# Kernel tuning notes

Hardware: AMD Instinct MI355X
Metric: run time of the kernel (lower is better)

## Reference

```python
import jax, jax.numpy as jnp
import numpy as np

B, S, D, H = 4, 1024, 1024, 16
HD = D // H  # head_dim = 64
NEG = -1e9  # stands in for float('-inf') in masked_fill; numerically safe


def setup_inputs() -> dict:
    key = jax.random.key(0)
    ks = jax.random.split(key, 8)
    q = jax.random.normal(ks[0], (B, S, D), dtype=jnp.float32)
    k = jax.random.normal(ks[1], (B, S, D), dtype=jnp.float32)
    v = jax.random.normal(ks[2], (B, S, D), dtype=jnp.float32)
    # padding mask: True marks padded positions; pad out the tail of each sequence
    pos = jnp.arange(S)
    lengths = jnp.array([S, S - 64, S - 128, S - 256])
    padding_mask = pos[None, :] >= lengths[:, None]  # [B, S] bool
    # additive causal mask: 0 on/below diagonal, NEG above
    causal_mask = jnp.where(jnp.tril(jnp.ones((S, S), dtype=bool)), 0.0, NEG).astype(jnp.float32)
    scale = 1.0 / np.sqrt(D)
    Wq = jax.random.normal(ks[3], (D, D), dtype=jnp.float32) * scale
    Wk = jax.random.normal(ks[4], (D, D), dtype=jnp.float32) * scale
    Wv = jax.random.normal(ks[5], (D, D), dtype=jnp.float32) * scale
    Wo = jax.random.normal(ks[6], (D, D), dtype=jnp.float32) * scale
    return {"q": q, "k": k, "v": v, "padding_mask": padding_mask,
            "causal_mask": causal_mask, "Wq": Wq, "Wk": Wk, "Wv": Wv,
            "Wo": Wo, "n_heads": H}


def reference(q, k, v, padding_mask, causal_mask, Wq, Wk, Wv, Wo, n_heads):
    b, s, d = q.shape
    hd = d // n_heads
    # projections (nn.Linear: x @ W^T, no bias)
    qp = (q @ Wq.T).reshape(b, s, n_heads, hd).transpose(0, 2, 1, 3)  # [b,h,s,hd]
    kp = (k @ Wk.T).reshape(b, s, n_heads, hd).transpose(0, 2, 1, 3)
    vp = (v @ Wv.T).reshape(b, s, n_heads, hd).transpose(0, 2, 1, 3)
    scores = jnp.einsum('bhqd,bhkd->bhqk', qp, kp) / jnp.sqrt(jnp.float32(hd))
    # masked_fill(padding_mask, -inf): mask broadcast over heads and query dim
    scores = jnp.where(padding_mask[:, None, None, :], NEG, scores)
    scores = scores + causal_mask  # additive causal mask
    attn = jax.nn.softmax(scores, axis=-1)
    out = jnp.einsum('bhqk,bhkd->bhqd', attn, vp)
    out = out.transpose(0, 2, 1, 3).reshape(b, s, d)
    return out @ Wo.T
```

## Files before the change

kernel.cpp:

```cpp
#include <hip/hip_runtime.h>
#include <hip/hip_bf16.h>

#define BB 4
#define SS 1024
#define DD 1024
#define HH 16
#define HD 64
#define MM (BB*SS)


typedef __bf16 bf16x8 __attribute__((ext_vector_type(8)));
typedef __bf16 bf16x4 __attribute__((ext_vector_type(4)));
typedef float  f32x4  __attribute__((ext_vector_type(4)));

__global__ __launch_bounds__(256) void expand_mask(const void* __restrict__ pmraw,
                                                   float* __restrict__ madd,
                                                   int n)
{
    const unsigned char* bytes = (const unsigned char*)pmraw;
    __shared__ int isbool;
    if (threadIdx.x == 0) isbool = 0;
    __syncthreads();
    int flag = 0;
    for (int idx = threadIdx.x; idx < n; idx += 256) {
        if ((idx & 3) && bytes[idx]) flag = 1;
    }
    if (flag) atomicOr(&isbool, 1);
    __syncthreads();
    int i = blockIdx.x * 256 + threadIdx.x;
    if (i < n) {
        int v = isbool ? (int)bytes[i] : ((const int*)pmraw)[i];
        madd[i] = (v != 0) ? -1e9f : 0.0f;
    }
}

__global__ __launch_bounds__(256) void convall(const float* __restrict__ q,
                                               const float* __restrict__ k,
                                               const float* __restrict__ v,
                                               const float* __restrict__ Wq,
                                               const float* __restrict__ Wk,
                                               const float* __restrict__ Wv,
                                               const float* __restrict__ Wo,
                                               __bf16* __restrict__ qb,
                                               __bf16* __restrict__ kb,
                                               __bf16* __restrict__ vb,
                                               __bf16* __restrict__ Wqb,
                                               __bf16* __restrict__ Wkb,
                                               __bf16* __restrict__ Wvb,
                                               __bf16* __restrict__ Wob)
{
    const float* s; __bf16* d; int i;
    if (blockIdx.y < 3) {
        if (blockIdx.y == 0)      { s = q; d = qb; }
        else if (blockIdx.y == 1) { s = k; d = kb; }
        else                      { s = v; d = vb; }
        i = (blockIdx.x * 256 + threadIdx.x) * 4;
    } else {
        const int wsel = blockIdx.x >> 10;
        const int lx   = blockIdx.x & 1023;
        if (wsel == 0)      { s = Wq; d = Wqb; }
        else if (wsel == 1) { s = Wk; d = Wkb; }
        else if (wsel == 2) { s = Wv; d = Wvb; }
        else                { s = Wo; d = Wob; }
        i = (lx * 256 + threadIdx.x) * 4;
    }
    float4 x = *(const float4*)(s + i);
    bf16x4 o;
    o[0] = (__bf16)x.x; o[1] = (__bf16)x.y;
    o[2] = (__bf16)x.z; o[3] = (__bf16)x.w;
    *(bf16x4*)(d + i) = o;
}

#define GM 128
#define GN 64
#define GK 64

__global__ __launch_bounds__(256) void gemm_qkv(const __bf16* __restrict__ qb,
                                                const __bf16* __restrict__ kb,
                                                const __bf16* __restrict__ vb,
                                                const __bf16* __restrict__ Wqb,
                                                const __bf16* __restrict__ Wkb,
                                                const __bf16* __restrict__ Wvb,
                                                __bf16* __restrict__ Qp,
                                                __bf16* __restrict__ Kp,
                                                __bf16* __restrict__ VpT)
{
    __shared__ __align__(16) __bf16 As[GM][GK];
    __shared__ __align__(16) __bf16 Bs[GN][GK];

    const __bf16 *A, *W; __bf16* C;
    const int z = blockIdx.z;
    if (z == 0)      { A = qb; W = Wqb; C = Qp;  }
    else if (z == 1) { A = kb; W = Wkb; C = Kp;  }
    else             { A = vb; W = Wvb; C = VpT; }

    const int tid  = threadIdx.x;
    const int lane = tid & 63;
    const int w    = tid >> 6;
    const int l15  = lane & 15;
    const int quad = lane >> 4;
    const int wr   = w >> 1;
    const int wc   = w & 1;

    const int m0 = blockIdx.x * GM;
    const int n0 = blockIdx.y * GN;

    const int srow = tid >> 3;
    const int scol = (tid & 7) * 8;
    const int gcol = (((tid & 7) ^ (srow & 7)) * 8);

    const __bf16* gA = A + (size_t)(m0 + srow) * DD + gcol;
    const __bf16* gB = W + (size_t)(n0 + srow) * DD + gcol;

    f32x4 acc[4][2] = {};

    for (int k0 = 0; k0 < DD; k0 += GK) {
        __syncthreads();
        #pragma unroll
        for (int c = 0; c < 4; ++c)
            __builtin_amdgcn_global_load_lds(
                (const __attribute__((address_space(1))) void*)(gA + (size_t)c * 32 * DD + k0),
                (__attribute__((address_space(3))) void*)(&As[c * 32 + srow][scol]), 16, 0, 0);
        #pragma unroll
        for (int c = 0; c < 2; ++c)
            __builtin_amdgcn_global_load_lds(
                (const __attribute__((address_space(1))) void*)(gB + (size_t)c * 32 * DD + k0),
                (__attribute__((address_space(3))) void*)(&Bs[c * 32 + srow][scol]), 16, 0, 0);
        __syncthreads();

        #pragma unroll
        for (int ks = 0; ks < 2; ++ks) {
            const int cidx = ((ks * 4 + quad) ^ (l15 & 7)) * 8;
            bf16x8 af[4], bf[2];
            #pragma unroll
            for (int mt = 0; mt < 4; ++mt)
                af[mt] = *(const bf16x8*)&As[wr * 64 + mt * 16 + l15][cidx];
            #pragma unroll
            for (int nt = 0; nt < 2; ++nt)
                bf[nt] = *(const bf16x8*)&Bs[wc * 32 + nt * 16 + l15][cidx];
            #pragma unroll
            for (int mt = 0; mt < 4; ++mt)
                #pragma unroll
                for (int nt = 0; nt < 2; ++nt)
                    acc[mt][nt] = __builtin_amdgcn_mfma_f32_16x16x32_bf16(
                        af[mt], bf[nt], acc[mt][nt], 0, 0, 0);
        }
    }

    if (z == 0) {
        #pragma unroll
        for (int mt = 0; mt < 4; ++mt)
            #pragma unroll
            for (int nt = 0; nt < 2; ++nt)
                #pragma unroll
                for (int r = 0; r < 4; ++r)
                    acc[mt][nt][r] *= 0.125f;
    }

    if (z == 2) {
        #pragma unroll
        for (int mt = 0; mt < 4; ++mt)
            #pragma unroll
            for (int nt = 0; nt < 2; ++nt) {
                bf16x4 o;
                #pragma unroll
                for (int r = 0; r < 4; ++r) o[r] = (__bf16)acc[mt][nt][r];
                const int n = n0 + wc * 32 + nt * 16 + l15;
                const int m = m0 + wr * 64 + mt * 16 + quad * 4;
                *(bf16x4*)&C[(size_t)n * MM + m] = o;
            }
    } else {
        #pragma unroll
        for (int mt = 0; mt < 4; ++mt)
            #pragma unroll
            for (int nt = 0; nt < 2; ++nt)
                #pragma unroll
                for (int r = 0; r < 4; ++r)
                    C[(size_t)(m0 + wr * 64 + mt * 16 + quad * 4 + r) * DD +
                      (n0 + wc * 32 + nt * 16 + l15)] = (__bf16)acc[mt][nt][r];
    }
}

__global__ __launch_bounds__(256) void gemm_wo(const __bf16* __restrict__ A,
                                               const __bf16* __restrict__ W,
                                               float* __restrict__ C)
{
    __shared__ __align__(16) __bf16 As[GM][GK];
    __shared__ __align__(16) __bf16 Bs[GN][GK];

    const int tid  = threadIdx.x;
    const int lane = tid & 63;
    const int w    = tid >> 6;
    const int l15  = lane & 15;
    const int quad = lane >> 4;
    const int wr   = w >> 1;
    const int wc   = w & 1;

    const int m0 = blockIdx.x * GM;
    const int n0 = blockIdx.y * GN;

    const int srow = tid >> 3;
    const int scol = (tid & 7) * 8;
    const int gcol = (((tid & 7) ^ (srow & 7)) * 8);

    const __bf16* gA = A + (size_t)(m0 + srow) * DD + gcol;
    const __bf16* gB = W + (size_t)(n0 + srow) * DD + gcol;

    f32x4 acc[4][2] = {};

    for (int k0 = 0; k0 < DD; k0 += GK) {
        __syncthreads();
        #pragma unroll
        for (int c = 0; c < 4; ++c)
            __builtin_amdgcn_global_load_lds(
                (const __attribute__((address_space(1))) void*)(gA + (size_t)c * 32 * DD + k0),
                (__attribute__((address_space(3))) void*)(&As[c * 32 + srow][scol]), 16, 0, 0);
        #pragma unroll
        for (int c = 0; c < 2; ++c)
            __builtin_amdgcn_global_load_lds(
                (const __attribute__((address_space(1))) void*)(gB + (size_t)c * 32 * DD + k0),
                (__attribute__((address_space(3))) void*)(&Bs[c * 32 + srow][scol]), 16, 0, 0);
        __syncthreads();

        #pragma unroll
        for (int ks = 0; ks < 2; ++ks) {
            const int cidx = ((ks * 4 + quad) ^ (l15 & 7)) * 8;
            bf16x8 af[4], bf[2];
            #pragma unroll
            for (int mt = 0; mt < 4; ++mt)
                af[mt] = *(const bf16x8*)&As[wr * 64 + mt * 16 + l15][cidx];
            #pragma unroll
            for (int nt = 0; nt < 2; ++nt)
                bf[nt] = *(const bf16x8*)&Bs[wc * 32 + nt * 16 + l15][cidx];
            #pragma unroll
            for (int mt = 0; mt < 4; ++mt)
                #pragma unroll
                for (int nt = 0; nt < 2; ++nt)
                    acc[mt][nt] = __builtin_amdgcn_mfma_f32_16x16x32_bf16(
                        af[mt], bf[nt], acc[mt][nt], 0, 0, 0);
        }
    }

    #pragma unroll
    for (int mt = 0; mt < 4; ++mt)
        #pragma unroll
        for (int nt = 0; nt < 2; ++nt)
            #pragma unroll
            for (int r = 0; r < 4; ++r)
                C[(size_t)(m0 + wr * 64 + mt * 16 + quad * 4 + r) * DD +
                  (n0 + wc * 32 + nt * 16 + l15)] = acc[mt][nt][r];
}

#define PSTR 72
#define OSTR 68

__global__ __launch_bounds__(256, 2) void flash_attn(const __bf16* __restrict__ Qp,
                                                     const __bf16* __restrict__ Kp,
                                                     const __bf16* __restrict__ VpT,
                                                     const float* __restrict__ maskadd,
                                                     __bf16* __restrict__ Op)
{
    __shared__ __align__(16) unsigned char smem[4 * 64 * PSTR * 2];
    __bf16 (*Pl)[64][PSTR]  = (__bf16 (*)[64][PSTR])smem;
    float  (*Obuf)[64][OSTR] = (float (*)[64][OSTR])smem;

    const int tid  = threadIdx.x;
    const int lane = tid & 63;
    const int w    = tid >> 6;
    const int l15  = lane & 15;
    const int quad = lane >> 4;
    const int h    = w & 1;
    const int tile = w >> 1;

    const int bh = blockIdx.x;
    const int hh = bh & (HH - 1);
    const int b  = bh >> 4;
    const int p  = blockIdx.y;
    const int m  = tile ? (15 - p) : p;

    const size_t hbase = (size_t)b * SS * DD + (size_t)hh * HD;
    const int q0 = m * 64;

    bf16x8 qf[4][2];
    #pragma unroll
    for (int qt = 0; qt < 4; ++qt) {
        const __bf16* qp = Qp + hbase + (size_t)(q0 + qt * 16 + l15) * DD + quad * 8;
        qf[qt][0] = *(const bf16x8*)qp;
        qf[qt][1] = *(const bf16x8*)(qp + 32);
    }

    const __bf16* vt = VpT + (size_t)(hh * HD) * MM + b * SS;
    const float* madd = maskadd + b * SS;

    f32x4 Ov[4][4] = {};
    float lsumq[4] = {};

    for (int kt = h; kt <= m; kt += 2) {
        const int kbase = kt * 64;
        const bool diag = (kt == m);

        f32x4 St[4][4];
        #pragma unroll
        for (int kg = 0; kg < 4; ++kg) {
            const __bf16* kp = Kp + hbase + (size_t)(kbase + kg * 16 + l15) * DD + quad * 8;
            bf16x8 kf0 = *(const bf16x8*)kp;
            bf16x8 kf1 = *(const bf16x8*)(kp + 32);
            #pragma unroll
            for (int qt = 0; qt < 4; ++qt) {
                f32x4 s = {};
                s = __builtin_amdgcn_mfma_f32_16x16x32_bf16(kf0, qf[qt][0], s, 0, 0, 0);
                s = __builtin_amdgcn_mfma_f32_16x16x32_bf16(kf1, qf[qt][1], s, 0, 0, 0);
                St[kg][qt] = s;
            }
        }

        #pragma unroll
        for (int kg = 0; kg < 4; ++kg) {
            const float4 mr = *(const float4*)&madd[kbase + kg * 16 + quad * 4];
            #pragma unroll
            for (int qt = 0; qt < 4; ++qt) {
                const int i = q0 + qt * 16 + l15;
                bf16x4 pk;
                #pragma unroll
                for (int r = 0; r < 4; ++r) {
                    const int j = kbase + kg * 16 + quad * 4 + r;
                    float pv = __expf(St[kg][qt][r] + ((const float*)&mr)[r]);
                    if (diag && j > i) pv = 0.f;
                    lsumq[qt] += pv;
                    pk[r] = (__bf16)pv;
                }
                *(bf16x4*)&Pl[w][qt * 16 + l15][kg * 16 + quad * 4] = pk;
            }
        }

        bf16x8 pf[4][2];
        #pragma unroll
        for (int qt = 0; qt < 4; ++qt) {
            pf[qt][0] = *(const bf16x8*)&Pl[w][qt * 16 + l15][quad * 8];
            pf[qt][1] = *(const bf16x8*)&Pl[w][qt * 16 + l15][quad * 8 + 32];
        }

        #pragma unroll
        for (int dt = 0; dt < 4; ++dt) {
            const __bf16* vp = vt + (size_t)(dt * 16 + l15) * MM + kbase + quad * 8;
            bf16x8 vf0 = *(const bf16x8*)vp;
            bf16x8 vf1 = *(const bf16x8*)(vp + 32);
            #pragma unroll
            for (int qt = 0; qt < 4; ++qt) {
                Ov[qt][dt] = __builtin_amdgcn_mfma_f32_16x16x32_bf16(pf[qt][0], vf0, Ov[qt][dt], 0, 0, 0);
                Ov[qt][dt] = __builtin_amdgcn_mfma_f32_16x16x32_bf16(pf[qt][1], vf1, Ov[qt][dt], 0, 0, 0);
            }
        }
    }

    #pragma unroll
    for (int off = 16; off < 64; off <<= 1)
        #pragma unroll
        for (int qt = 0; qt < 4; ++qt)
            lsumq[qt] += __shfl_xor(lsumq[qt], off);

    __syncthreads();
    if (h == 1) {
        #pragma unroll
        for (int qt = 0; qt < 4; ++qt) {
            #pragma unroll
            for (int dt = 0; dt < 4; ++dt)
                #pragma unroll
                for (int r = 0; r < 4; ++r)
                    Obuf[tile][qt * 16 + quad * 4 + r][dt * 16 + l15] = Ov[qt][dt][r];
            if (quad == 0)
                Obuf[tile][qt * 16 + l15][64] = lsumq[qt];
        }
    }
    __syncthreads();
    if (h == 0) {
        #pragma unroll
        for (int qt = 0; qt < 4; ++qt) {
            const float rcp = 1.0f / (lsumq[qt] + Obuf[tile][qt * 16 + l15][64]);
            float rq[4];
            #pragma unroll
            for (int r = 0; r < 4; ++r) rq[r] = __shfl(rcp, quad * 4 + r);
            #pragma unroll
            for (int dt = 0; dt < 4; ++dt)
                #pragma unroll
                for (int r = 0; r < 4; ++r) {
                    const int i = q0 + qt * 16 + quad * 4 + r;
                    float o = Ov[qt][dt][r] +
                              Obuf[tile][qt * 16 + quad * 4 + r][dt * 16 + l15];
                    Op[hbase + (size_t)i * DD + dt * 16 + l15] = (__bf16)(o * rq[r]);
                }
        }
    }
}

extern "C" void kernel_launch(void* const* d_in, const int* in_sizes, int n_in,
                              void* d_out, int out_size, void* d_ws, size_t ws_size,
                              hipStream_t stream)
{
    const float* q  = (const float*)d_in[0];
    const float* k  = (const float*)d_in[1];
    const float* v  = (const float*)d_in[2];
    const void*  pm = d_in[3];
    const float* Wq = (const float*)d_in[5];
    const float* Wk = (const float*)d_in[6];
    const float* Wv = (const float*)d_in[7];
    const float* Wo = (const float*)d_in[8];

    char* ws = (char*)d_ws;
    float* madd = (float*)ws;
    const size_t MB = 1024 * 1024;
    char* base = ws + 65536;

    __bf16* qb  = (__bf16*)(base +  0 * MB);
    __bf16* kb  = (__bf16*)(base +  8 * MB);
    __bf16* vb  = (__bf16*)(base + 16 * MB);
    __bf16* Wqb = (__bf16*)(base + 24 * MB);
    __bf16* Wkb = (__bf16*)(base + 26 * MB);
    __bf16* Wvb = (__bf16*)(base + 28 * MB);
    __bf16* Wob = (__bf16*)(base + 30 * MB);
    __bf16* Qp  = (__bf16*)(base + 32 * MB);
    __bf16* Kp  = (__bf16*)(base + 40 * MB);
    __bf16* VpT = (__bf16*)(base + 48 * MB);
    __bf16* Op  = qb;

    float* out = (float*)d_out;
    const int NT = MM * DD;

    expand_mask<<<(BB * SS) / 256, 256, 0, stream>>>(pm, madd, BB * SS);
    convall<<<dim3(NT / 1024, 4), 256, 0, stream>>>(q, k, v, Wq, Wk, Wv, Wo,
                                                    qb, kb, vb, Wqb, Wkb, Wvb, Wob);

    dim3 gg(MM / GM, DD / GN, 3);
    gemm_qkv<<<gg, 256, 0, stream>>>(qb, kb, vb, Wqb, Wkb, Wvb, Qp, Kp, VpT);

    dim3 ga(BB * HH, 8);
    flash_attn<<<ga, 256, 0, stream>>>(Qp, Kp, VpT, madd, Op);

    dim3 gw(MM / GM, DD / GN);
    gemm_wo<<<gw, 256, 0, stream>>>(Op, Wob, out);
}
```

Measured before the change: 212.3 us.

## Double-buffer LDS tiles in projection GEMMs to overlap loads with MFMA

```diff
diff --git a/kernel.cpp b/kernel.cpp
--- a/kernel.cpp
+++ b/kernel.cpp
@@ -74,6 +74,42 @@
 #define GM 128
 #define GN 64
 #define GK 64
+#define KSTEPS (DD / GK)
+
+#define STAGE(As, Bs, buf, k0)                                                          \
+    {                                                                                   \
+        _Pragma("unroll")                                                               \
+        for (int c = 0; c < 4; ++c)                                                     \
+            __builtin_amdgcn_global_load_lds(                                           \
+                (const __attribute__((address_space(1))) void*)(gA + (size_t)c * 32 * DD + (k0)), \
+                (__attribute__((address_space(3))) void*)(&As[buf][c * 32 + srow][scol]), 16, 0, 0); \
+        _Pragma("unroll")                                                               \
+        for (int c = 0; c < 2; ++c)                                                     \
+            __builtin_amdgcn_global_load_lds(                                           \
+                (const __attribute__((address_space(1))) void*)(gB + (size_t)c * 32 * DD + (k0)), \
+                (__attribute__((address_space(3))) void*)(&Bs[buf][c * 32 + srow][scol]), 16, 0, 0); \
+    }
+
+#define COMPUTE(As, Bs, buf)                                                            \
+    {                                                                                   \
+        _Pragma("unroll")                                                               \
+        for (int ks = 0; ks < 2; ++ks) {                                                \
+            const int cidx = ((ks * 4 + quad) ^ (l15 & 7)) * 8;                         \
+            bf16x8 af[4], bf[2];                                                        \
+            _Pragma("unroll")                                                           \
+            for (int mt = 0; mt < 4; ++mt)                                              \
+                af[mt] = *(const bf16x8*)&As[buf][wr * 64 + mt * 16 + l15][cidx];       \
+            _Pragma("unroll")                                                           \
+            for (int nt = 0; nt < 2; ++nt)                                              \
+                bf[nt] = *(const bf16x8*)&Bs[buf][wc * 32 + nt * 16 + l15][cidx];       \
+            _Pragma("unroll")                                                           \
+            for (int mt = 0; mt < 4; ++mt)                                              \
+                _Pragma("unroll")                                                       \
+                for (int nt = 0; nt < 2; ++nt)                                          \
+                    acc[mt][nt] = __builtin_amdgcn_mfma_f32_16x16x32_bf16(              \
+                        af[mt], bf[nt], acc[mt][nt], 0, 0, 0);                          \
+        }                                                                               \
+    }
 
 __global__ __launch_bounds__(256) void gemm_qkv(const __bf16* __restrict__ qb,
                                                 const __bf16* __restrict__ kb,
@@ -85,8 +121,8 @@
                                                 __bf16* __restrict__ Kp,
                                                 __bf16* __restrict__ VpT)
 {
-    __shared__ __align__(16) __bf16 As[GM][GK];
-    __shared__ __align__(16) __bf16 Bs[GN][GK];
+    __shared__ __align__(16) __bf16 As[2][GM][GK];
+    __shared__ __align__(16) __bf16 Bs[2][GN][GK];
 
     const __bf16 *A, *W; __bf16* C;
     const int z = blockIdx.z;
@@ -114,37 +150,15 @@
 
     f32x4 acc[4][2] = {};
 
-    for (int k0 = 0; k0 < DD; k0 += GK) {
+    STAGE(As, Bs, 0, 0);
+    __syncthreads();
+    for (int t = 0; t < KSTEPS; t += 2) {
+        STAGE(As, Bs, 1, (t + 1) * GK);
+        COMPUTE(As, Bs, 0);
         __syncthreads();
-        #pragma unroll
-        for (int c = 0; c < 4; ++c)
-            __builtin_amdgcn_global_load_lds(
-                (const __attribute__((address_space(1))) void*)(gA + (size_t)c * 32 * DD + k0),
-                (__attribute__((address_space(3))) void*)(&As[c * 32 + srow][scol]), 16, 0, 0);
-        #pragma unroll
-        for (int c = 0; c < 2; ++c)
-            __builtin_amdgcn_global_load_lds(
-                (const __attribute__((address_space(1))) void*)(gB + (size_t)c * 32 * DD + k0),
-                (__attribute__((address_space(3))) void*)(&Bs[c * 32 + srow][scol]), 16, 0, 0);
+        if (t + 2 < KSTEPS) STAGE(As, Bs, 0, (t + 2) * GK);
+        COMPUTE(As, Bs, 1);
         __syncthreads();
-
-        #pragma unroll
-        for (int ks = 0; ks < 2; ++ks) {
-            const int cidx = ((ks * 4 + quad) ^ (l15 & 7)) * 8;
-            bf16x8 af[4], bf[2];
-            #pragma unroll
-            for (int mt = 0; mt < 4; ++mt)
-                af[mt] = *(const bf16x8*)&As[wr * 64 + mt * 16 + l15][cidx];
-            #pragma unroll
-            for (int nt = 0; nt < 2; ++nt)
-                bf[nt] = *(const bf16x8*)&Bs[wc * 32 + nt * 16 + l15][cidx];
-            #pragma unroll
-            for (int mt = 0; mt < 4; ++mt)
-                #pragma unroll
-                for (int nt = 0; nt < 2; ++nt)
-                    acc[mt][nt] = __builtin_amdgcn_mfma_f32_16x16x32_bf16(
-                        af[mt], bf[nt], acc[mt][nt], 0, 0, 0);
-        }
     }
 
     if (z == 0) {
@@ -181,12 +195,12 @@
     }
 }
 
-__global__ __launch_bounds__(256) void gemm_wo(const __bf16* __restrict__ A,
+__global__ __launch_bounds__(256) void gemm_wo(const __bf16* __restrict__ Ain,
                                                const __bf16* __restrict__ W,
                                                float* __restrict__ C)
 {
-    __shared__ __align__(16) __bf16 As[GM][GK];
-    __shared__ __align__(16) __bf16 Bs[GN][GK];
+    __shared__ __align__(16) __bf16 As[2][GM][GK];
+    __shared__ __align__(16) __bf16 Bs[2][GN][GK];
 
     const int tid  = threadIdx.x;
     const int lane = tid & 63;
@@ -203,42 +217,20 @@
     const int scol = (tid & 7) * 8;
     const int gcol = (((tid & 7) ^ (srow & 7)) * 8);
 
-    const __bf16* gA = A + (size_t)(m0 + srow) * DD + gcol;
-    const __bf16* gB = W + (size_t)(n0 + srow) * DD + gcol;
+    const __bf16* gA = Ain + (size_t)(m0 + srow) * DD + gcol;
+    const __bf16* gB = W   + (size_t)(n0 + srow) * DD + gcol;
 
     f32x4 acc[4][2] = {};
 
-    for (int k0 = 0; k0 < DD; k0 += GK) {
+    STAGE(As, Bs, 0, 0);
+    __syncthreads();
+    for (int t = 0; t < KSTEPS; t += 2) {
+        STAGE(As, Bs, 1, (t + 1) * GK);
+        COMPUTE(As, Bs, 0);
         __syncthreads();
-        #pragma unroll
-        for (int c = 0; c < 4; ++c)
-            __builtin_amdgcn_global_load_lds(
-                (const __attribute__((address_space(1))) void*)(gA + (size_t)c * 32 * DD + k0),
-                (__attribute__((address_space(3))) void*)(&As[c * 32 + srow][scol]), 16, 0, 0);
-        #pragma unroll
-        for (int c = 0; c < 2; ++c)
-            __builtin_amdgcn_global_load_lds(
-                (const __attribute__((address_space(1))) void*)(gB + (size_t)c * 32 * DD + k0),
-                (__attribute__((address_space(3))) void*)(&Bs[c * 32 + srow][scol]), 16, 0, 0);
+        if (t + 2 < KSTEPS) STAGE(As, Bs, 0, (t + 2) * GK);
+        COMPUTE(As, Bs, 1);
         __syncthreads();
-
-        #pragma unroll
-        for (int ks = 0; ks < 2; ++ks) {
-            const int cidx = ((ks * 4 + quad) ^ (l15 & 7)) * 8;
-            bf16x8 af[4], bf[2];
-            #pragma unroll
-            for (int mt = 0; mt < 4; ++mt)
-                af[mt] = *(const bf16x8*)&As[wr * 64 + mt * 16 + l15][cidx];
-            #pragma unroll
-            for (int nt = 0; nt < 2; ++nt)
-                bf[nt] = *(const bf16x8*)&Bs[wc * 32 + nt * 16 + l15][cidx];
-            #pragma unroll
-            for (int mt = 0; mt < 4; ++mt)
-                #pragma unroll
-                for (int nt = 0; nt < 2; ++nt)
-                    acc[mt][nt] = __builtin_amdgcn_mfma_f32_16x16x32_bf16(
-                        af[mt], bf[nt], acc[mt][nt], 0, 0, 0);
-        }
     }
 
     #pragma unroll
```

After: 220.4 us. 3.8% more time.

## Split each query tile's KV loop across four waves and double attention grid

Applied to the files above, without the earlier changes.

```diff
diff --git a/kernel.cpp b/kernel.cpp
--- a/kernel.cpp
+++ b/kernel.cpp
@@ -254,14 +254,14 @@
 #define PSTR 72
 #define OSTR 68
 
-__global__ __launch_bounds__(256, 2) void flash_attn(const __bf16* __restrict__ Qp,
+__global__ __launch_bounds__(256, 4) void flash_attn(const __bf16* __restrict__ Qp,
                                                      const __bf16* __restrict__ Kp,
                                                      const __bf16* __restrict__ VpT,
                                                      const float* __restrict__ maskadd,
                                                      __bf16* __restrict__ Op)
 {
     __shared__ __align__(16) unsigned char smem[4 * 64 * PSTR * 2];
-    __bf16 (*Pl)[64][PSTR]  = (__bf16 (*)[64][PSTR])smem;
+    __bf16 (*Pl)[64][PSTR]   = (__bf16 (*)[64][PSTR])smem;
     float  (*Obuf)[64][OSTR] = (float (*)[64][OSTR])smem;
 
     const int tid  = threadIdx.x;
@@ -269,14 +269,11 @@
     const int w    = tid >> 6;
     const int l15  = lane & 15;
     const int quad = lane >> 4;
-    const int h    = w & 1;
-    const int tile = w >> 1;
 
     const int bh = blockIdx.x;
     const int hh = bh & (HH - 1);
     const int b  = bh >> 4;
-    const int p  = blockIdx.y;
-    const int m  = tile ? (15 - p) : p;
+    const int m  = blockIdx.y;
 
     const size_t hbase = (size_t)b * SS * DD + (size_t)hh * HD;
     const int q0 = m * 64;
@@ -295,7 +292,7 @@
     f32x4 Ov[4][4] = {};
     float lsumq[4] = {};
 
-    for (int kt = h; kt <= m; kt += 2) {
+    for (int kt = w; kt <= m; kt += 4) {
         const int kbase = kt * 64;
         const bool diag = (kt == m);
 
@@ -360,23 +357,48 @@
             lsumq[qt] += __shfl_xor(lsumq[qt], off);
 
     __syncthreads();
-    if (h == 1) {
+    if (w >= 2) {
         #pragma unroll
         for (int qt = 0; qt < 4; ++qt) {
             #pragma unroll
             for (int dt = 0; dt < 4; ++dt)
                 #pragma unroll
                 for (int r = 0; r < 4; ++r)
-                    Obuf[tile][qt * 16 + quad * 4 + r][dt * 16 + l15] = Ov[qt][dt][r];
+                    Obuf[w - 2][qt * 16 + quad * 4 + r][dt * 16 + l15] = Ov[qt][dt][r];
             if (quad == 0)
-                Obuf[tile][qt * 16 + l15][64] = lsumq[qt];
-        }
-    }
-    __syncthreads();
-    if (h == 0) {
+                Obuf[w - 2][qt * 16 + l15][64] = lsumq[qt];
+        }
+    }
+    __syncthreads();
+    if (w < 2) {
         #pragma unroll
         for (int qt = 0; qt < 4; ++qt) {
-            const float rcp = 1.0f / (lsumq[qt] + Obuf[tile][qt * 16 + l15][64]);
+            lsumq[qt] += Obuf[w][qt * 16 + l15][64];
+            #pragma unroll
+            for (int dt = 0; dt < 4; ++dt)
+                #pragma unroll
+                for (int r = 0; r < 4; ++r)
+                    Ov[qt][dt][r] += Obuf[w][qt * 16 + quad * 4 + r][dt * 16 + l15];
+        }
+    }
+    __syncthreads();
+    if (w == 1) {
+        #pragma unroll
+        for (int qt = 0; qt < 4; ++qt) {
+            #pragma unroll
+            for (int dt = 0; dt < 4; ++dt)
+                #pragma unroll
+                for (int r = 0; r < 4; ++r)
+                    Obuf[0][qt * 16 + quad * 4 + r][dt * 16 + l15] = Ov[qt][dt][r];
+            if (quad == 0)
+                Obuf[0][qt * 16 + l15][64] = lsumq[qt];
+        }
+    }
+    __syncthreads();
+    if (w == 0) {
+        #pragma unroll
+        for (int qt = 0; qt < 4; ++qt) {
+            const float rcp = 1.0f / (lsumq[qt] + Obuf[0][qt * 16 + l15][64]);
             float rq[4];
             #pragma unroll
             for (int r = 0; r < 4; ++r) rq[r] = __shfl(rcp, quad * 4 + r);
@@ -386,7 +408,7 @@
                 for (int r = 0; r < 4; ++r) {
                     const int i = q0 + qt * 16 + quad * 4 + r;
                     float o = Ov[qt][dt][r] +
-                              Obuf[tile][qt * 16 + quad * 4 + r][dt * 16 + l15];
+                              Obuf[0][qt * 16 + quad * 4 + r][dt * 16 + l15];
                     Op[hbase + (size_t)i * DD + dt * 16 + l15] = (__bf16)(o * rq[r]);
                 }
         }
@@ -433,7 +455,7 @@
     dim3 gg(MM / GM, DD / GN, 3);
     gemm_qkv<<<gg, 256, 0, stream>>>(qb, kb, vb, Wqb, Wkb, Wvb, Qp, Kp, VpT);
 
-    dim3 ga(BB * HH, 8);
+    dim3 ga(BB * HH, 16);
     flash_attn<<<ga, 256, 0, stream>>>(Qp, Kp, VpT, madd, Op);
 
     dim3 gw(MM / GM, DD / GN);
```

After: 262.7 us. 1.24x slower.
